# Kernel tuning notes

Hardware: AMD Instinct MI355X
Metric: run time of the kernel (lower is better)

The kernel has to match this reference:

```python
import jax, jax.numpy as jnp
import numpy as np

B, T, D_IN = 32, 512, 1024
D_HID = 512
D_CODE = 1024
K = 256  # codebook size
COMMIT = 0.25
LAMBDA_MMD = 0.5
LN_EPS = 1e-5


def setup_inputs() -> dict:
    key = jax.random.key(0)
    ks = jax.random.split(key, 20)
    def w(k, shape, scale=0.02):
        return jax.random.normal(k, shape, dtype=jnp.float32) * scale
    inp = {
        "x": jax.random.normal(ks[0], (B, T, D_IN), dtype=jnp.float32),
        "prior": jax.random.normal(ks[1], (B, D_CODE), dtype=jnp.float32),
        # encoder: Linear(1024,512) -> LN(512) -> ReLU -> Linear(512,1024)
        "enc_W1": w(ks[2], (D_IN, D_HID)), "enc_b1": jnp.zeros((D_HID,), jnp.float32),
        "ln_g": jnp.ones((D_HID,), jnp.float32), "ln_b": jnp.zeros((D_HID,), jnp.float32),
        "enc_W2": w(ks[3], (D_HID, D_CODE)), "enc_b2": jnp.zeros((D_CODE,), jnp.float32),
        # codebook, init uniform(-1/K, 1/K) like the torch module
        "codebook": jax.random.uniform(ks[4], (K, D_CODE), jnp.float32, -1.0 / K, 1.0 / K),
        # projector: Linear(1024,512) -> ReLU -> Linear(512,1024)
        "proj_W1": w(ks[5], (D_CODE, D_HID)), "proj_b1": jnp.zeros((D_HID,), jnp.float32),
        "proj_W2": w(ks[6], (D_HID, D_CODE)), "proj_b2": jnp.zeros((D_CODE,), jnp.float32),
        # GRU(1024 -> 1024), torch gate order (r, z, n)
        "gru_Wih": w(ks[7], (D_CODE, 3 * D_CODE)), "gru_Whh": w(ks[8], (D_CODE, 3 * D_CODE)),
        "gru_bih": jnp.zeros((3 * D_CODE,), jnp.float32), "gru_bhh": jnp.zeros((3 * D_CODE,), jnp.float32),
        # head: Linear(1024, 1024)
        "head_W": w(ks[9], (D_CODE, D_IN)), "head_b": jnp.zeros((D_IN,), jnp.float32),
    }
    return inp


def _gaussian_kernel(a, b):
    # exp(-cdist(a,b)^2 / dim)
    d = a.shape[1]
    sq = (jnp.sum(a * a, 1, keepdims=True) + jnp.sum(b * b, 1)[None, :]
          - 2.0 * a @ b.T)
    sq = jnp.maximum(sq, 0.0)
    return jnp.exp(-sq / d)


def _gru(quantized, Wih, Whh, bih, bhh):
    # quantized: [B, T, D]; precompute input projections, scan over time
    gx = jnp.einsum("btd,de->bte", quantized, Wih) + bih  # [B,T,3D]
    gx = jnp.swapaxes(gx, 0, 1)  # [T,B,3D]
    h0 = jnp.zeros((quantized.shape[0], Whh.shape[0]), quantized.dtype)

    def step(h, gxt):
        gh = h @ Whh + bhh
        xr, xz, xn = jnp.split(gxt, 3, axis=-1)
        hr, hz, hn = jnp.split(gh, 3, axis=-1)
        r = jax.nn.sigmoid(xr + hr)
        z = jax.nn.sigmoid(xz + hz)
        n = jnp.tanh(xn + r * hn)
        h_new = (1.0 - z) * n + z * h
        return h_new, h_new

    _, hs = jax.lax.scan(step, h0, gx)  # [T,B,D]
    return jnp.swapaxes(hs, 0, 1)  # [B,T,D]


def reference(x, prior, enc_W1, enc_b1, ln_g, ln_b, enc_W2, enc_b2, codebook,
              proj_W1, proj_b1, proj_W2, proj_b2,
              gru_Wih, gru_Whh, gru_bih, gru_bhh, head_W, head_b):
    # ---- encoder ----
    h = x @ enc_W1 + enc_b1
    mu = jnp.mean(h, -1, keepdims=True)
    var = jnp.mean((h - mu) ** 2, -1, keepdims=True)
    h = (h - mu) * jax.lax.rsqrt(var + LN_EPS) * ln_g + ln_b
    h = jax.nn.relu(h)
    features = h @ enc_W2 + enc_b2  # [B,T,D_CODE]

    # ---- vector quantizer ----
    flat = features.reshape(-1, D_CODE)  # [B*T, D]
    dist = (jnp.sum(flat * flat, 1, keepdims=True) + jnp.sum(codebook * codebook, 1)
            - 2.0 * flat @ codebook.T)  # [B*T, K]
    idx = jnp.argmin(dist, axis=1)  # [B*T]
    quantized = codebook[idx].reshape(features.shape)
    e_latent = jnp.mean((jax.lax.stop_gradient(quantized) - features) ** 2)
    q_latent = jnp.mean((quantized - jax.lax.stop_gradient(features)) ** 2)
    vq_loss = q_latent + COMMIT * e_latent
    quantized = features + jax.lax.stop_gradient(quantized - features)  # straight-through

    # ---- projector + MMD ----
    p = jax.nn.relu(quantized @ proj_W1 + proj_b1)
    aligned = p @ proj_W2 + proj_b2  # [B,T,D]
    xm = jnp.mean(aligned, axis=1)  # [B,D]
    xx = _gaussian_kernel(xm, xm).mean()
    yy = _gaussian_kernel(prior, prior).mean()
    xy = _gaussian_kernel(xm, prior).mean()
    mmd = xx + yy - 2.0 * xy

    # ---- GRU decoder + head ----
    context = _gru(quantized, gru_Wih, gru_Whh, gru_bih, gru_bhh)
    recon = context @ head_W + head_b  # [B,T,D_IN]
    recon_loss = jnp.mean((recon - x) ** 2)

    total = recon_loss + vq_loss + LAMBDA_MMD * mmd
    return jnp.stack([recon_loss, vq_loss, mmd, total])
```

## Files before the change

kernel.cpp:

```cpp
#include <hip/hip_runtime.h>


typedef __attribute__((ext_vector_type(4))) float  f32x4;
typedef __attribute__((ext_vector_type(8))) short  s16x8;
typedef __attribute__((ext_vector_type(4))) short  s16x4;
typedef __attribute__((ext_vector_type(8))) __bf16 bf16x8;
typedef unsigned long long u64;
typedef unsigned int       u32;

__device__ __forceinline__ short f2bf(float f) {
  __bf16 h = (__bf16)f;
  return __builtin_bit_cast(short, h);
}
__device__ __forceinline__ float bf2f(short s) {
  return (float)__builtin_bit_cast(__bf16, s);
}
__device__ __forceinline__ f32x4 mfma16(s16x8 a, s16x8 b, f32x4 c) {
  return __builtin_amdgcn_mfma_f32_16x16x32_bf16(
      __builtin_bit_cast(bf16x8, a), __builtin_bit_cast(bf16x8, b), c, 0, 0, 0);
}
__device__ __forceinline__ void vm_drain() {
  asm volatile("s_waitcnt vmcnt(0)" ::: "memory");
}
__device__ __forceinline__ u64 ld_uc64(const u64* p) {
  return __hip_atomic_load(p, __ATOMIC_RELAXED, __HIP_MEMORY_SCOPE_AGENT);
}
__device__ __forceinline__ void st_uc32(u32* p, u32 v) {
  __hip_atomic_store(p, v, __ATOMIC_RELAXED, __HIP_MEMORY_SCOPE_AGENT);
}

template<bool AF32, int EPI>
__global__ __launch_bounds__(256)
void gemm_k(const void* __restrict__ Ap, const float* __restrict__ Bp,
            const float* __restrict__ bias, void* __restrict__ Cp,
            const float* __restrict__ Xref, float* __restrict__ accum,
            int M, int N, int K)
{
  __shared__ short As[128][72];
  __shared__ short Bs[128][72];
  const int tid  = threadIdx.x;
  const long bm  = (long)blockIdx.x * 128;
  const long bn  = (long)blockIdx.y * 128;
  const int wave = tid >> 6, lane = tid & 63;
  const int wm = (wave >> 1) * 64, wn = (wave & 1) * 64;
  const int l16 = lane & 15, quad = lane >> 4;

  f32x4 acc[4][4];
#pragma unroll
  for (int i = 0; i < 4; ++i)
#pragma unroll
    for (int j = 0; j < 4; ++j) acc[i][j] = (f32x4){0.f, 0.f, 0.f, 0.f};

  const int atc = tid & 15, atr = tid >> 4;
  const int btc = tid & 31, btr = tid >> 5;

  for (int kt = 0; kt < K; kt += 64) {
#pragma unroll
    for (int p = 0; p < 8; ++p) {
      int r = p * 16 + atr;
      if (AF32) {
        const float* src = (const float*)Ap + (bm + r) * (long)K + kt + atc * 4;
        f32x4 v = *(const f32x4*)src;
        s16x4 s;
        s.x = f2bf(v.x); s.y = f2bf(v.y); s.z = f2bf(v.z); s.w = f2bf(v.w);
        *(s16x4*)&As[r][atc * 4] = s;
      } else {
        const short* src = (const short*)Ap + (bm + r) * (long)K + kt + atc * 4;
        *(s16x4*)&As[r][atc * 4] = *(const s16x4*)src;
      }
    }
#pragma unroll
    for (int p = 0; p < 8; ++p) {
      int kk = p * 8 + btr;
      const float* brow = Bp + (long)(kt + kk) * N + bn + btc;
#pragma unroll
      for (int j = 0; j < 4; ++j) Bs[btc + 32 * j][kk] = f2bf(brow[32 * j]);
    }
    __syncthreads();
#pragma unroll
    for (int kk = 0; kk < 64; kk += 32) {
      s16x8 af[4], bf[4];
#pragma unroll
      for (int i = 0; i < 4; ++i)
        af[i] = *(const s16x8*)&As[wm + i * 16 + l16][kk + quad * 8];
#pragma unroll
      for (int j = 0; j < 4; ++j)
        bf[j] = *(const s16x8*)&Bs[wn + j * 16 + l16][kk + quad * 8];
#pragma unroll
      for (int i = 0; i < 4; ++i)
#pragma unroll
        for (int j = 0; j < 4; ++j) acc[i][j] = mfma16(af[i], bf[j], acc[i][j]);
    }
    __syncthreads();
  }

  if (EPI == 3) {
    float ls = 0.f;
#pragma unroll
    for (int i = 0; i < 4; ++i)
#pragma unroll
      for (int j = 0; j < 4; ++j) {
        long col = bn + wn + j * 16 + l16;
        float bv = bias[col];
#pragma unroll
        for (int r = 0; r < 4; ++r) {
          long row = bm + wm + i * 16 + quad * 4 + r;
          float v = acc[i][j][r] + bv;
          float d = v - Xref[row * N + col];
          ls += d * d;
        }
      }
#pragma unroll
    for (int off = 32; off > 0; off >>= 1) ls += __shfl_xor(ls, off, 64);
    if (lane == 0) atomicAdd(accum, ls);
  } else {
#pragma unroll
    for (int i = 0; i < 4; ++i)
#pragma unroll
      for (int j = 0; j < 4; ++j) {
        long col = bn + wn + j * 16 + l16;
        float bv = bias[col];
#pragma unroll
        for (int r = 0; r < 4; ++r) {
          long row = bm + wm + i * 16 + quad * 4 + r;
          float v = acc[i][j][r] + bv;
          if (EPI == 2) v = fmaxf(v, 0.f);
          if (EPI == 0) ((float*)Cp)[row * N + col] = v;
          else          ((short*)Cp)[row * N + col] = f2bf(v);
        }
      }
  }
}

__global__ __launch_bounds__(256)
void ln_relu_k(const float* __restrict__ hp, const float* __restrict__ g,
               const float* __restrict__ b, short* __restrict__ out)
{
  const int wave = threadIdx.x >> 6, lane = threadIdx.x & 63;
  const long row = (long)blockIdx.x * 4 + wave;
  const float* hr = hp + row * 512;
  const int c0 = lane * 4, c1 = 256 + lane * 4;
  f32x4 v0 = *(const f32x4*)(hr + c0);
  f32x4 v1 = *(const f32x4*)(hr + c1);
  float s  = v0.x + v0.y + v0.z + v0.w + v1.x + v1.y + v1.z + v1.w;
  float ss = v0.x*v0.x + v0.y*v0.y + v0.z*v0.z + v0.w*v0.w
           + v1.x*v1.x + v1.y*v1.y + v1.z*v1.z + v1.w*v1.w;
#pragma unroll
  for (int off = 32; off > 0; off >>= 1) {
    s  += __shfl_xor(s, off, 64);
    ss += __shfl_xor(ss, off, 64);
  }
  float mu  = s * (1.f / 512.f);
  float var = ss * (1.f / 512.f) - mu * mu;
  float rs  = rsqrtf(var + 1e-5f);
  f32x4 g0 = *(const f32x4*)(g + c0), bb0 = *(const f32x4*)(b + c0);
  f32x4 g1 = *(const f32x4*)(g + c1), bb1 = *(const f32x4*)(b + c1);
  s16x4 o0, o1;
#pragma unroll
  for (int e = 0; e < 4; ++e) {
    o0[e] = f2bf(fmaxf((v0[e] - mu) * rs * g0[e] + bb0[e], 0.f));
    o1[e] = f2bf(fmaxf((v1[e] - mu) * rs * g1[e] + bb1[e], 0.f));
  }
  *(s16x4*)(out + row * 512 + c0) = o0;
  *(s16x4*)(out + row * 512 + c1) = o1;
}

__global__ __launch_bounds__(256)
void prep_cb_k(const float* __restrict__ cb, float* __restrict__ cbT,
               float* __restrict__ cbBias)
{
  __shared__ float red[256];
  const int r = blockIdx.x, tid = threadIdx.x;
  const float* row = cb + (long)r * 1024;
  float ss = 0.f;
  for (int c = tid; c < 1024; c += 256) {
    float v = row[c];
    cbT[(long)c * 256 + r] = v;
    ss += v * v;
  }
  red[tid] = ss; __syncthreads();
  for (int st = 128; st > 0; st >>= 1) {
    if (tid < st) red[tid] += red[tid + st];
    __syncthreads();
  }
  if (tid == 0) cbBias[r] = -0.5f * red[0];
}

__global__ __launch_bounds__(256)
void vq_k(const float* __restrict__ sc, const short* __restrict__ feat,
          int* __restrict__ idxp, float* __restrict__ e_acc)
{
  __shared__ float ep[4];
  const int wave = threadIdx.x >> 6, lane = threadIdx.x & 63;
  const long row = (long)blockIdx.x * 4 + wave;
  f32x4 s = *(const f32x4*)(sc + row * 256 + lane * 4);
  float best = s.x; int bi = lane * 4;
  if (s.y > best) { best = s.y; bi = lane * 4 + 1; }
  if (s.z > best) { best = s.z; bi = lane * 4 + 2; }
  if (s.w > best) { best = s.w; bi = lane * 4 + 3; }
#pragma unroll
  for (int off = 32; off > 0; off >>= 1) {
    float ov = __shfl_xor(best, off, 64);
    int   oi = __shfl_xor(bi, off, 64);
    if (ov > best || (ov == best && oi < bi)) { best = ov; bi = oi; }
  }
  const short* fr = feat + row * 1024;
  float sq = 0.f;
#pragma unroll
  for (int p = 0; p < 2; ++p) {
    s16x8 v = *(const s16x8*)(fr + p * 512 + lane * 8);
#pragma unroll
    for (int e = 0; e < 8; ++e) { float f = bf2f(v[e]); sq += f * f; }
  }
#pragma unroll
  for (int off = 32; off > 0; off >>= 1) sq += __shfl_xor(sq, off, 64);
  if (lane == 0) { idxp[row] = bi; ep[wave] = sq - 2.f * best; }
  __syncthreads();
  if (threadIdx.x == 0) atomicAdd(e_acc, ep[0] + ep[1] + ep[2] + ep[3]);
}

__global__ __launch_bounds__(256)
void hist_xm_k(const int* __restrict__ idxp, const float* __restrict__ AC,
               float* __restrict__ xm)
{
  __shared__ int   hist[256];
  __shared__ float hf[256];
  const int b = blockIdx.x, tid = threadIdx.x;
  hist[tid] = 0; __syncthreads();
  for (int t = tid; t < 512; t += 256) atomicAdd(&hist[idxp[b * 512 + t]], 1);
  __syncthreads();
  hf[tid] = (float)hist[tid] * (1.f / 512.f);
  __syncthreads();
  for (int d = tid; d < 1024; d += 256) {
    float a = 0.f;
    for (int k = 0; k < 256; ++k) a += hf[k] * AC[(long)k * 1024 + d];
    xm[(long)b * 1024 + d] = a;
  }
}

__global__ __launch_bounds__(1024)
void mmd_k(const float* __restrict__ xm, const float* __restrict__ prior,
           float* __restrict__ mmd_out)
{
  extern __shared__ float xs[];
  __shared__ float red[48];
  const int tid = threadIdx.x;
  for (int i = tid; i < 32 * 1024; i += 1024)
    xs[(i >> 10) * 1028 + (i & 1023)] = xm[i];
  __syncthreads();
  const int i = tid >> 5, j = tid & 31;
  const float* xi = xs + i * 1028;
  const float* xj = xs + j * 1028;
  const float* pi = prior + (long)i * 1024;
  const float* pj = prior + (long)j * 1024;
  float dxx = 0.f, dyy = 0.f, dxy = 0.f;
  for (int d = 0; d < 1024; d += 4) {
    f32x4 a = *(const f32x4*)(xi + d);
    f32x4 b = *(const f32x4*)(xj + d);
    f32x4 p = *(const f32x4*)(pi + d);
    f32x4 q = *(const f32x4*)(pj + d);
#pragma unroll
    for (int e = 0; e < 4; ++e) {
      float t1 = a[e] - b[e]; dxx += t1 * t1;
      float t2 = p[e] - q[e]; dyy += t2 * t2;
      float t3 = a[e] - q[e]; dxy += t3 * t3;
    }
  }
  float kxx = __expf(-dxx * (1.f / 1024.f));
  float kyy = __expf(-dyy * (1.f / 1024.f));
  float kxy = __expf(-dxy * (1.f / 1024.f));
  const int wv = tid >> 6, lane = tid & 63;
#pragma unroll
  for (int off = 32; off > 0; off >>= 1) {
    kxx += __shfl_xor(kxx, off, 64);
    kyy += __shfl_xor(kyy, off, 64);
    kxy += __shfl_xor(kxy, off, 64);
  }
  if (lane == 0) { red[wv] = kxx; red[16 + wv] = kyy; red[32 + wv] = kxy; }
  __syncthreads();
  if (tid == 0) {
    float sxx = 0.f, syy = 0.f, sxy = 0.f;
    for (int w = 0; w < 16; ++w) {
      sxx += red[w]; syy += red[16 + w]; sxy += red[32 + w];
    }
    mmd_out[0] = (sxx + syy - 2.f * sxy) * (1.f / 1024.f);
  }
}

__global__ __launch_bounds__(128, 1)
void gru_k(const float* __restrict__ Whh, const float* __restrict__ bhh,
           const float* __restrict__ cgx, const int* __restrict__ idxp,
           u32* __restrict__ hbuf, u32* __restrict__ ctx,
           int* __restrict__ flags)
{
  extern __shared__ short Bsl[];
  const int tid = threadIdx.x, g = blockIdx.x;
  const int wave = tid >> 6, lane = tid & 63;
  const int l16 = lane & 15, quad = lane >> 4;

  for (int i = tid; i < 48 * 1024; i += 128) {
    int c = i % 48, k = i / 48;
    int gate = c >> 4, dl = c & 15;
    Bsl[c * 1032 + k] = f2bf(Whh[(long)k * 3072 + gate * 1024 + g * 16 + dl]);
  }
  const int dcol = g * 16 + l16;
  const float bhr = bhh[dcol], bhz = bhh[dcol + 1024], bhn = bhh[dcol + 2048];
  const short* b0 = &Bsl[l16 * 1032 + quad * 8];
  const short* b1 = b0 + 16 * 1032;
  const short* b2 = b0 + 32 * 1032;
  const int arowbase = (wave * 16 + l16) * 512 + quad * 4;
  float hreg[4] = {0.f, 0.f, 0.f, 0.f};
  int brow[4];
#pragma unroll
  for (int r = 0; r < 4; ++r) brow[r] = wave * 16 + quad * 4 + r;
  const int myflag = g * 2 + wave;
  __syncthreads();

  float xr[4], xz[4], xn[4];
#pragma unroll
  for (int r = 0; r < 4; ++r) {
    int code = idxp[brow[r] * 512];
    const float* gp = cgx + (long)code * 3072 + dcol;
    xr[r] = gp[0]; xz[r] = gp[1024]; xn[r] = gp[2048];
  }

  for (int t = 0; t < 512; ++t) {
    if (t > 0) {
      int a, b;
      do {
        a = __hip_atomic_load(&flags[lane],      __ATOMIC_RELAXED,
                              __HIP_MEMORY_SCOPE_AGENT);
        b = __hip_atomic_load(&flags[64 + lane], __ATOMIC_RELAXED,
                              __HIP_MEMORY_SCOPE_AGENT);
      } while (__any(a < t || b < t));
    }
    const u64* ap = (const u64*)(hbuf + ((t & 1) << 14) + arowbase);
    f32x4 ar_ = {0.f,0.f,0.f,0.f}, az = ar_, an = ar_;
#pragma unroll 8
    for (int ks = 0; ks < 32; ++ks) {
      u64 q0 = ld_uc64(ap + ks * 8);
      u64 q1 = ld_uc64(ap + ks * 8 + 1);
      union { u64 q[2]; s16x8 v; } ua; ua.q[0] = q0; ua.q[1] = q1;
      s16x8 vr = *(const s16x8*)(b0 + ks * 32);
      s16x8 vz = *(const s16x8*)(b1 + ks * 32);
      s16x8 vn = *(const s16x8*)(b2 + ks * 32);
      ar_ = mfma16(ua.v, vr, ar_);
      az  = mfma16(ua.v, vz, az);
      an  = mfma16(ua.v, vn, an);
    }
#pragma unroll
    for (int r = 0; r < 4; ++r) {
      float rr = 1.f / (1.f + __expf(-(xr[r] + ar_[r] + bhr)));
      float zz = 1.f / (1.f + __expf(-(xz[r] + az[r] + bhz)));
      float u  = xn[r] + rr * (an[r] + bhn);
      float e  = __expf(-2.f * u);
      float nn = (1.f - e) / (1.f + e);
      hreg[r]  = (1.f - zz) * nn + zz * hreg[r];
    }
    int tn = (t + 1 < 512) ? t + 1 : 0;
#pragma unroll
    for (int r = 0; r < 4; ++r) {
      int code = idxp[brow[r] * 512 + tn];
      const float* gp = cgx + (long)code * 3072 + dcol;
      xr[r] = gp[0]; xz[r] = gp[1024]; xn[r] = gp[2048];
    }
    u32* hdst = hbuf + (((t + 1) & 1) << 14);
#pragma unroll
    for (int r = 0; r < 4; ++r) {
      unsigned short hb = (unsigned short)f2bf(hreg[r]);
      u32 other = (u32)__shfl_xor((int)hb, 1, 64) & 0xffffu;
      if ((l16 & 1) == 0) {
        u32 w = (u32)hb | (other << 16);
        st_uc32(hdst + brow[r] * 512 + (dcol >> 1), w);
        ctx[((long)brow[r] * 512 + t) * 512 + (dcol >> 1)] = w;
      }
    }
    vm_drain();
    if (lane == 0)
      __hip_atomic_store(&flags[myflag], t + 1, __ATOMIC_RELAXED,
                         __HIP_MEMORY_SCOPE_AGENT);
  }
}

__global__ void fin_k(const float* __restrict__ scal, float* __restrict__ out)
{
  float recon = scal[3] * (1.f / 16777216.f);
  float vq    = 1.25f * scal[2] * (1.f / 16777216.f);
  float mmd   = scal[4];
  out[0] = recon;
  out[1] = vq;
  out[2] = mmd;
  out[3] = recon + vq + 0.5f * mmd;
}

extern "C" void kernel_launch(void* const* d_in, const int* in_sizes, int n_in,
                              void* d_out, int out_size, void* d_ws, size_t ws_size,
                              hipStream_t stream)
{
  const float* x     = (const float*)d_in[0];
  const float* prior = (const float*)d_in[1];
  const float* encW1 = (const float*)d_in[2];
  const float* encb1 = (const float*)d_in[3];
  const float* lng   = (const float*)d_in[4];
  const float* lnb   = (const float*)d_in[5];
  const float* encW2 = (const float*)d_in[6];
  const float* encb2 = (const float*)d_in[7];
  const float* cb    = (const float*)d_in[8];
  const float* pW1   = (const float*)d_in[9];
  const float* pb1   = (const float*)d_in[10];
  const float* pW2   = (const float*)d_in[11];
  const float* pb2   = (const float*)d_in[12];
  const float* Wih   = (const float*)d_in[13];
  const float* Whh   = (const float*)d_in[14];
  const float* bih   = (const float*)d_in[15];
  const float* bhh   = (const float*)d_in[16];
  const float* headW = (const float*)d_in[17];
  const float* headb = (const float*)d_in[18];

  char* ws = (char*)d_ws;
  if (ws_size < 89654528) return;
  float* h_pre  = (float*)(ws + 0);
  float* scores = h_pre;
  u32*   hbuf   = (u32*)(ws + 0);
  int*   flags  = (int*)(ws + 131072);
  short* h1     = (short*)(ws + 33554432);
  short* feat   = (short*)(ws + 50331648);
  u32*   ctx    = (u32*)feat;
  float* cgx    = (float*)(ws + 83886080);
  float* AC     = (float*)(ws + 87031808);
  float* cbT    = (float*)(ws + 88080384);
  short* ch     = (short*)(ws + 89128960);
  float* xm     = (float*)(ws + 89391104);
  int*   idxp   = (int*)  (ws + 89522176);
  float* scal   = (float*)(ws + 89653248);
  float* e_acc  = scal + 2;
  float* r_acc  = scal + 3;
  float* mmdv   = scal + 4;
  float* cbBias = (float*)(ws + 89653504);

  hipMemsetAsync(scal, 0, 256, stream);

  dim3 blk(256);
  prep_cb_k<<<256, blk, 0, stream>>>(cb, cbT, cbBias);
  gemm_k<true, 0><<<dim3(128, 4), blk, 0, stream>>>(
      x, encW1, encb1, h_pre, nullptr, nullptr, 16384, 512, 1024);
  ln_relu_k<<<4096, blk, 0, stream>>>(h_pre, lng, lnb, h1);
  gemm_k<false, 1><<<dim3(128, 8), blk, 0, stream>>>(
      h1, encW2, encb2, feat, nullptr, nullptr, 16384, 1024, 512);
  gemm_k<false, 0><<<dim3(128, 2), blk, 0, stream>>>(
      feat, cbT, cbBias, scores, nullptr, nullptr, 16384, 256, 1024);
  vq_k<<<4096, blk, 0, stream>>>(scores, feat, idxp, e_acc);
  hipMemsetAsync(ws, 0, 131072 + 512, stream);
  gemm_k<true, 2><<<dim3(2, 4), blk, 0, stream>>>(
      cb, pW1, pb1, ch, nullptr, nullptr, 256, 512, 1024);
  gemm_k<false, 0><<<dim3(2, 8), blk, 0, stream>>>(
      ch, pW2, pb2, AC, nullptr, nullptr, 256, 1024, 512);
  gemm_k<true, 0><<<dim3(2, 24), blk, 0, stream>>>(
      cb, Wih, bih, cgx, nullptr, nullptr, 256, 3072, 1024);
  hist_xm_k<<<32, blk, 0, stream>>>(idxp, AC, xm);
  mmd_k<<<1, 1024, 32 * 1028 * 4, stream>>>(xm, prior, mmdv);
  gru_k<<<64, 128, 48 * 1032 * 2, stream>>>(Whh, bhh, cgx, idxp, hbuf, ctx, flags);
  gemm_k<false, 3><<<dim3(128, 8), blk, 0, stream>>>(
      ctx, headW, headb, nullptr, x, r_acc, 16384, 1024, 1024);
  fin_k<<<1, 1, 0, stream>>>(scal, (float*)d_out);
}
```

Baseline: 5.740 ms.

## Read GRU hidden state from ctx buffer and keep r/z weights in registers

The GRU kernel drops the separate double-buffered hidden-state array and reads the previous step's hidden state straight from the context output buffer using nontemporal vector loads. The h0=0 step skips the matmul entirely. The r and z gate weight fragments are preloaded into registers once, so only the n-gate fragment is read from LDS each step. The LDS row stride is padded from 1032 to 1034. The aim is to shorten the latency-bound serial recurrence, at the cost of heavy register pressure and reliance on nontemporal loads seeing other blocks' relaxed atomic stores.

```diff
diff --git a/kernel.cpp b/kernel.cpp
--- a/kernel.cpp
+++ b/kernel.cpp
@@ -21,9 +21,6 @@
 }
 __device__ __forceinline__ void vm_drain() {
   asm volatile("s_waitcnt vmcnt(0)" ::: "memory");
-}
-__device__ __forceinline__ u64 ld_uc64(const u64* p) {
-  return __hip_atomic_load(p, __ATOMIC_RELAXED, __HIP_MEMORY_SCOPE_AGENT);
 }
 __device__ __forceinline__ void st_uc32(u32* p, u32 v) {
   __hip_atomic_store(p, v, __ATOMIC_RELAXED, __HIP_MEMORY_SCOPE_AGENT);
@@ -290,7 +287,7 @@
 __global__ __launch_bounds__(128, 1)
 void gru_k(const float* __restrict__ Whh, const float* __restrict__ bhh,
            const float* __restrict__ cgx, const int* __restrict__ idxp,
-           u32* __restrict__ hbuf, u32* __restrict__ ctx,
+           u32* __restrict__ ctxw, const short* __restrict__ ctxr,
            int* __restrict__ flags)
 {
   extern __shared__ short Bsl[];
@@ -301,20 +298,28 @@
   for (int i = tid; i < 48 * 1024; i += 128) {
     int c = i % 48, k = i / 48;
     int gate = c >> 4, dl = c & 15;
-    Bsl[c * 1032 + k] = f2bf(Whh[(long)k * 3072 + gate * 1024 + g * 16 + dl]);
+    Bsl[c * 1034 + k] = f2bf(Whh[(long)k * 3072 + gate * 1024 + g * 16 + dl]);
   }
   const int dcol = g * 16 + l16;
   const float bhr = bhh[dcol], bhz = bhh[dcol + 1024], bhn = bhh[dcol + 2048];
-  const short* b0 = &Bsl[l16 * 1032 + quad * 8];
-  const short* b1 = b0 + 16 * 1032;
-  const short* b2 = b0 + 32 * 1032;
-  const int arowbase = (wave * 16 + l16) * 512 + quad * 4;
+  const short* b0 = &Bsl[l16 * 1034 + quad * 8];
+  const short* b1 = b0 + 16 * 1034;
+  const short* b2 = b0 + 32 * 1034;
   float hreg[4] = {0.f, 0.f, 0.f, 0.f};
   int brow[4];
 #pragma unroll
   for (int r = 0; r < 4; ++r) brow[r] = wave * 16 + quad * 4 + r;
   const int myflag = g * 2 + wave;
   __syncthreads();
+
+  s16x8 br[32], bz[32];
+#pragma unroll
+  for (int ks = 0; ks < 32; ++ks) {
+    br[ks] = *(const s16x8*)(b0 + ks * 32);
+    bz[ks] = *(const s16x8*)(b1 + ks * 32);
+  }
+
+  const long arow = ((long)(wave * 16 + l16) * 512) * 1024 + quad * 8;
 
   float xr[4], xz[4], xn[4];
 #pragma unroll
@@ -325,6 +330,7 @@
   }
 
   for (int t = 0; t < 512; ++t) {
+    f32x4 ar_ = {0.f,0.f,0.f,0.f}, az = ar_, an = ar_;
     if (t > 0) {
       int a, b;
       do {
@@ -333,20 +339,15 @@
         b = __hip_atomic_load(&flags[64 + lane], __ATOMIC_RELAXED,
                               __HIP_MEMORY_SCOPE_AGENT);
       } while (__any(a < t || b < t));
-    }
-    const u64* ap = (const u64*)(hbuf + ((t & 1) << 14) + arowbase);
-    f32x4 ar_ = {0.f,0.f,0.f,0.f}, az = ar_, an = ar_;
-#pragma unroll 8
-    for (int ks = 0; ks < 32; ++ks) {
-      u64 q0 = ld_uc64(ap + ks * 8);
-      u64 q1 = ld_uc64(ap + ks * 8 + 1);
-      union { u64 q[2]; s16x8 v; } ua; ua.q[0] = q0; ua.q[1] = q1;
-      s16x8 vr = *(const s16x8*)(b0 + ks * 32);
-      s16x8 vz = *(const s16x8*)(b1 + ks * 32);
-      s16x8 vn = *(const s16x8*)(b2 + ks * 32);
-      ar_ = mfma16(ua.v, vr, ar_);
-      az  = mfma16(ua.v, vz, az);
-      an  = mfma16(ua.v, vn, an);
+      asm volatile("" ::: "memory");
+      const short* ap = ctxr + arow + (long)(t - 1) * 1024;
+#pragma unroll
+      for (int ks = 0; ks < 32; ++ks) {
+        s16x8 a8 = __builtin_nontemporal_load((const s16x8*)(ap + ks * 32));
+        ar_ = mfma16(a8, br[ks], ar_);
+        az  = mfma16(a8, bz[ks], az);
+        an  = mfma16(a8, *(const s16x8*)(b2 + ks * 32), an);
+      }
     }
 #pragma unroll
     for (int r = 0; r < 4; ++r) {
@@ -364,15 +365,13 @@
       const float* gp = cgx + (long)code * 3072 + dcol;
       xr[r] = gp[0]; xz[r] = gp[1024]; xn[r] = gp[2048];
     }
-    u32* hdst = hbuf + (((t + 1) & 1) << 14);
 #pragma unroll
     for (int r = 0; r < 4; ++r) {
       unsigned short hb = (unsigned short)f2bf(hreg[r]);
       u32 other = (u32)__shfl_xor((int)hb, 1, 64) & 0xffffu;
       if ((l16 & 1) == 0) {
         u32 w = (u32)hb | (other << 16);
-        st_uc32(hdst + brow[r] * 512 + (dcol >> 1), w);
-        ctx[((long)brow[r] * 512 + t) * 512 + (dcol >> 1)] = w;
+        st_uc32(ctxw + ((long)brow[r] * 512 + t) * 512 + (dcol >> 1), w);
       }
     }
     vm_drain();
@@ -421,11 +420,11 @@
   if (ws_size < 89654528) return;
   float* h_pre  = (float*)(ws + 0);
   float* scores = h_pre;
-  u32*   hbuf   = (u32*)(ws + 0);
   int*   flags  = (int*)(ws + 131072);
   short* h1     = (short*)(ws + 33554432);
   short* feat   = (short*)(ws + 50331648);
-  u32*   ctx    = (u32*)feat;
+  u32*   ctxw   = (u32*)feat;
+  short* ctxr   = feat;
   float* cgx    = (float*)(ws + 83886080);
   float* AC     = (float*)(ws + 87031808);
   float* cbT    = (float*)(ws + 88080384);
@@ -450,7 +449,7 @@
   gemm_k<false, 0><<<dim3(128, 2), blk, 0, stream>>>(
       feat, cbT, cbBias, scores, nullptr, nullptr, 16384, 256, 1024);
   vq_k<<<4096, blk, 0, stream>>>(scores, feat, idxp, e_acc);
-  hipMemsetAsync(ws, 0, 131072 + 512, stream);
+  hipMemsetAsync(flags, 0, 512, stream);
   gemm_k<true, 2><<<dim3(2, 4), blk, 0, stream>>>(
       cb, pW1, pb1, ch, nullptr, nullptr, 256, 512, 1024);
   gemm_k<false, 0><<<dim3(2, 8), blk, 0, stream>>>(
@@ -459,8 +458,9 @@
       cb, Wih, bih, cgx, nullptr, nullptr, 256, 3072, 1024);
   hist_xm_k<<<32, blk, 0, stream>>>(idxp, AC, xm);
   mmd_k<<<1, 1024, 32 * 1028 * 4, stream>>>(xm, prior, mmdv);
-  gru_k<<<64, 128, 48 * 1032 * 2, stream>>>(Whh, bhh, cgx, idxp, hbuf, ctx, flags);
+  gru_k<<<64, 128, 48 * 1034 * 2, stream>>>(Whh, bhh, cgx, idxp,
+                                            ctxw, ctxr, flags);
   gemm_k<false, 3><<<dim3(128, 8), blk, 0, stream>>>(
-      ctx, headW, headb, nullptr, x, r_acc, 16384, 1024, 1024);
+      ctxr, headW, headb, nullptr, x, r_acc, 16384, 1024, 1024);
   fin_k<<<1, 1, 0, stream>>>(scal, (float*)d_out);
 }
```

Result: slower. 8.439 ms (+47.0%).
